# Kernel tuning notes

Measured on AMD Instinct MI355X. Metric: run time of the kernel, lower is better.

Reference implementation:

```python
import jax, jax.numpy as jnp
import numpy as np

N_NODES = 50000
N_EDGES = 800000
D = 256
VOCAB = 50000
N_ETYPES = 3
N_STEPS = 5
N_GRAPHS = 64


def setup_inputs() -> dict:
    key = jax.random.key(0)
    ks = jax.random.split(key, 16)
    s = 1.0 / np.sqrt(D)
    return {
        "x": jax.random.randint(ks[0], (N_NODES,), 0, VOCAB),
        "src": jax.random.randint(ks[1], (N_EDGES,), 0, N_NODES),
        "dst": jax.random.randint(ks[2], (N_EDGES,), 0, N_NODES),
        "etypes": jax.random.randint(ks[3], (N_EDGES,), 0, N_ETYPES),
        "seg_ids": jnp.sort(jax.random.randint(ks[4], (N_NODES,), 0, N_GRAPHS)),
        "num_graphs": N_GRAPHS,
        "emb": jax.random.normal(ks[5], (VOCAB, D), jnp.float32),
        "W_msg": jax.random.normal(ks[6], (N_ETYPES, D, D), jnp.float32) * s,
        "b_msg": jax.random.normal(ks[7], (N_ETYPES, D), jnp.float32) * s,
        "w_ih": jax.random.normal(ks[8], (3 * D, D), jnp.float32) * s,
        "w_hh": jax.random.normal(ks[9], (3 * D, D), jnp.float32) * s,
        "b_ih": jax.random.normal(ks[10], (3 * D,), jnp.float32) * s,
        "b_hh": jax.random.normal(ks[11], (3 * D,), jnp.float32) * s,
        "gate_w": jax.random.normal(ks[12], (D, 1), jnp.float32) * s,
        "gate_b": jax.random.normal(ks[13], (1,), jnp.float32) * s,
    }


def _gru_cell(a, h, w_ih, w_hh, b_ih, b_hh):
    # a, h: [N, D]; gates: [N, 3D]
    gi = a @ w_ih.T + b_ih
    gh = h @ w_hh.T + b_hh
    i_r, i_z, i_n = jnp.split(gi, 3, axis=-1)
    h_r, h_z, h_n = jnp.split(gh, 3, axis=-1)
    r = jax.nn.sigmoid(i_r + h_r)
    z = jax.nn.sigmoid(i_z + h_z)
    n = jnp.tanh(i_n + r * h_n)
    return (1.0 - z) * n + z * h


def reference(x, src, dst, etypes, seg_ids, num_graphs, emb, W_msg, b_msg,
              w_ih, w_hh, b_ih, b_hh, gate_w, gate_b):
    # Embedding lookup (dropout is identity in eval mode)
    h = emb[x]  # [N, D]

    # GatedGraphConv: n_steps of per-etype linear message + scatter-add + GRU
    for _ in range(N_STEPS):
        # per-node transform under every etype's weight: [n_etypes, N, D]
        t = jnp.einsum("nd,edf->enf", h, W_msg)
        msg = t[etypes, src] + b_msg[etypes]        # [E, D]
        a = jax.ops.segment_sum(msg, dst, num_segments=N_NODES)  # [N, D]
        h = _gru_cell(a, h, w_ih, w_hh, b_ih, b_hh)

    # GlobalAttentionPooling: gate score + segment softmax + weighted sum
    gate = (h @ gate_w + gate_b)[:, 0]  # [N]
    gmax = jax.ops.segment_max(gate, seg_ids, num_segments=num_graphs)
    e = jnp.exp(gate - gmax[seg_ids])
    denom = jax.ops.segment_sum(e, seg_ids, num_segments=num_graphs)
    alpha = e / denom[seg_ids]  # [N]
    out = jax.ops.segment_sum(h * alpha[:, None], seg_ids, num_segments=num_graphs)
    return out  # [num_graphs, D]
```

## Files before the change

### kernel.cpp

```cpp
#include <hip/hip_runtime.h>
#include <hip/hip_bf16.h>
#include <stdint.h>

#define N_NODESC 50000
#define NPAD     50048
#define N_EDGESC 800000
#define DIM      256
#define DIM3     768
#define NSTEPS   5
#define NGRAPH   64

typedef __attribute__((ext_vector_type(4))) float  f32x4;
typedef __attribute__((ext_vector_type(8))) short  short8;
typedef __attribute__((ext_vector_type(4))) unsigned short u16x4;
typedef __attribute__((ext_vector_type(4))) _Float16 f16x4;

__device__ float          g_hf[(size_t)NPAD * DIM];
__device__ unsigned short g_hb[(size_t)NPAD * DIM];
__device__ unsigned short g_p [(size_t)NPAD * DIM3];
__device__ unsigned short g_a [(size_t)NPAD * DIM];
__device__ _Float16       g_gi[(size_t)NPAD * DIM3];
__device__ _Float16       g_gh[(size_t)NPAD * DIM3];
__device__ unsigned short g_Wc[DIM * DIM3];
__device__ unsigned short g_WI[DIM3 * DIM];
__device__ unsigned short g_WH[DIM3 * DIM];
__device__ int            g_cnt[NPAD * 4];
__device__ int            g_rowoff[N_NODESC + 1];
__device__ int            g_cur[N_NODESC];
__device__ unsigned       g_eidx[N_EDGESC];
__device__ int            g_bsum[256];
__device__ int            g_boff[256];
__device__ float          g_gate[N_NODESC];
__device__ int            g_soff[NGRAPH + 1];
__device__ float          g_gmax[NGRAPH];
__device__ float          g_gden[NGRAPH];

__device__ __forceinline__ float bf2f(unsigned short u) {
  unsigned x = ((unsigned)u) << 16;
  return __builtin_bit_cast(float, x);
}
__device__ __forceinline__ unsigned short f2bf(float f) {
  unsigned u = __builtin_bit_cast(unsigned, f);
  u += 0x7fffu + ((u >> 16) & 1u);
  return (unsigned short)(u >> 16);
}
__device__ __forceinline__ float sigm(float x) { return 1.0f / (1.0f + expf(-x)); }

__device__ __forceinline__ void async16(const void* g, void* l) {
  __builtin_amdgcn_global_load_lds(
      (const __attribute__((address_space(1))) unsigned int*)g,
      (__attribute__((address_space(3))) unsigned int*)l, 16, 0, 0);
}


__global__ void k_zero_cnt() {
  int i = blockIdx.x * 256 + threadIdx.x;
  g_cnt[i] = 0;
}

__global__ void k_prep_w(const float* __restrict__ Wmsg, const float* __restrict__ wih,
                         const float* __restrict__ whh) {
  int i = blockIdx.x * 256 + threadIdx.x;
  if (i < 196608) {
    int f = i / 768, j = i - f * 768;
    int e = j >> 8, d = j & 255;
    g_Wc[i] = f2bf(Wmsg[(e << 16) + (d << 8) + f]);
  } else if (i < 393216) {
    int t = i - 196608;
    g_WI[t] = f2bf(wih[t]);
  } else if (i < 589824) {
    int t = i - 393216;
    g_WH[t] = f2bf(whh[t]);
  }
}

__global__ void k_embed(const int* __restrict__ x, const float* __restrict__ emb) {
  int i = blockIdx.x * 256 + threadIdx.x;
  int n = i >> 6, t = i & 63;
  if (n >= N_NODESC) return;
  float4 v = *(const float4*)(emb + (size_t)x[n] * DIM + t * 4);
  *(float4*)(g_hf + (size_t)n * DIM + t * 4) = v;
  u16x4 b = {f2bf(v.x), f2bf(v.y), f2bf(v.z), f2bf(v.w)};
  *(u16x4*)(g_hb + (size_t)n * DIM + t * 4) = b;
}

__global__ void k_count(const int* __restrict__ dst, const int* __restrict__ et) {
  int e = blockIdx.x * 256 + threadIdx.x;
  if (e >= N_EDGESC) return;
  atomicAdd(&g_cnt[dst[e] * 4 + et[e]], 1);
}

__global__ void k_scan1() {
  __shared__ int lds[256];
  int n = blockIdx.x * 256 + threadIdx.x;
  int deg = (n < N_NODESC) ? (g_cnt[n * 4] + g_cnt[n * 4 + 1] + g_cnt[n * 4 + 2]) : 0;
  lds[threadIdx.x] = deg;
  __syncthreads();
  for (int o = 128; o > 0; o >>= 1) {
    if (threadIdx.x < o) lds[threadIdx.x] += lds[threadIdx.x + o];
    __syncthreads();
  }
  if (threadIdx.x == 0) g_bsum[blockIdx.x] = lds[0];
}

__global__ void k_scan2() {
  __shared__ int lds[256];
  int t = threadIdx.x;
  int v = (t < 196) ? g_bsum[t] : 0;
  lds[t] = v;
  __syncthreads();
  for (int o = 1; o < 256; o <<= 1) {
    int u = (t >= o) ? lds[t - o] : 0;
    __syncthreads();
    lds[t] += u;
    __syncthreads();
  }
  if (t < 196) g_boff[t] = lds[t] - v;
}

__global__ void k_scan3() {
  __shared__ int lds[256];
  int n = blockIdx.x * 256 + threadIdx.x;
  int t = threadIdx.x;
  int deg = (n < N_NODESC) ? (g_cnt[n * 4] + g_cnt[n * 4 + 1] + g_cnt[n * 4 + 2]) : 0;
  lds[t] = deg;
  __syncthreads();
  for (int o = 1; o < 256; o <<= 1) {
    int u = (t >= o) ? lds[t - o] : 0;
    __syncthreads();
    lds[t] += u;
    __syncthreads();
  }
  if (n < N_NODESC) {
    int off = g_boff[blockIdx.x] + lds[t] - deg;
    g_rowoff[n] = off;
    g_cur[n] = off;
  }
  if (n == N_NODESC - 1) g_rowoff[N_NODESC] = g_boff[blockIdx.x] + lds[t];
}

__global__ void k_fill(const int* __restrict__ src, const int* __restrict__ dst,
                       const int* __restrict__ et) {
  int e = blockIdx.x * 256 + threadIdx.x;
  if (e >= N_EDGESC) return;
  int p = atomicAdd(&g_cur[dst[e]], 1);
  g_eidx[p] = (((unsigned)src[e]) << 2) | (unsigned)et[e];
}

__global__ void k_segoff(const int* __restrict__ seg) {
  int n = blockIdx.x * 256 + threadIdx.x;
  if (n >= N_NODESC) return;
  int g = seg[n];
  int gp = (n == 0) ? -1 : seg[n - 1];
  for (int t = gp + 1; t <= g; ++t) g_soff[t] = n;
  if (n == N_NODESC - 1)
    for (int t = g + 1; t <= NGRAPH; ++t) g_soff[t] = N_NODESC;
}


#define ACC_ET(hv, et)                                                        \
  {                                                                           \
    float x0 = bf2f(hv[0]), x1 = bf2f(hv[1]), x2 = bf2f(hv[2]), x3 = bf2f(hv[3]); \
    if (et == 0)      { a0[0] += x0; a0[1] += x1; a0[2] += x2; a0[3] += x3; } \
    else if (et == 1) { a1[0] += x0; a1[1] += x1; a1[2] += x2; a1[3] += x3; } \
    else              { a2[0] += x0; a2[1] += x1; a2[2] += x2; a2[3] += x3; } \
  }

__global__ __launch_bounds__(256) void k_agg() {
  int node = blockIdx.x * 4 + (threadIdx.x >> 6);
  int lane = threadIdx.x & 63;
  if (node >= N_NODESC) return;
  float a0[4] = {0.f, 0.f, 0.f, 0.f};
  float a1[4] = {0.f, 0.f, 0.f, 0.f};
  float a2[4] = {0.f, 0.f, 0.f, 0.f};
  int s = g_rowoff[node], e = g_rowoff[node + 1];
  int i = s;
  for (; i + 4 <= e; i += 4) {
    unsigned v0 = g_eidx[i], v1 = g_eidx[i + 1], v2 = g_eidx[i + 2], v3 = g_eidx[i + 3];
    u16x4 hv0 = *(const u16x4*)(g_hb + (size_t)(v0 >> 2) * DIM + lane * 4);
    u16x4 hv1 = *(const u16x4*)(g_hb + (size_t)(v1 >> 2) * DIM + lane * 4);
    u16x4 hv2 = *(const u16x4*)(g_hb + (size_t)(v2 >> 2) * DIM + lane * 4);
    u16x4 hv3 = *(const u16x4*)(g_hb + (size_t)(v3 >> 2) * DIM + lane * 4);
    int e0 = (int)(v0 & 3u), e1 = (int)(v1 & 3u), e2 = (int)(v2 & 3u), e3 = (int)(v3 & 3u);
    ACC_ET(hv0, e0);
    ACC_ET(hv1, e1);
    ACC_ET(hv2, e2);
    ACC_ET(hv3, e3);
  }
  for (; i < e; ++i) {
    unsigned v = g_eidx[i];
    u16x4 hv = *(const u16x4*)(g_hb + (size_t)(v >> 2) * DIM + lane * 4);
    int et = (int)(v & 3u);
    ACC_ET(hv, et);
  }
  size_t base = (size_t)node * DIM3 + lane * 4;
  u16x4 o0 = {f2bf(a0[0]), f2bf(a0[1]), f2bf(a0[2]), f2bf(a0[3])};
  u16x4 o1 = {f2bf(a1[0]), f2bf(a1[1]), f2bf(a1[2]), f2bf(a1[3])};
  u16x4 o2 = {f2bf(a2[0]), f2bf(a2[1]), f2bf(a2[2]), f2bf(a2[3])};
  *(u16x4*)(g_p + base)       = o0;
  *(u16x4*)(g_p + base + 256) = o1;
  *(u16x4*)(g_p + base + 512) = o2;
}

template <int MODE>
__global__ __launch_bounds__(256) void k_gemm(const float* __restrict__ bias,
                                              const float* __restrict__ bmsg) {
  constexpr int K  = (MODE == 0) ? DIM3 : DIM;
  constexpr int NC = (MODE == 0) ? DIM : DIM3;
  const unsigned short* __restrict__ A  = (MODE == 0) ? g_p  : (MODE == 1) ? g_a  : g_hb;
  const unsigned short* __restrict__ BT = (MODE == 0) ? g_Wc : (MODE == 1) ? g_WI : g_WH;

  __shared__ unsigned short lA[128 * 64];
  __shared__ unsigned short lB[128 * 64];
  const int tx = threadIdx.x;
  const int lane = tx & 63;
  const int wave = tx >> 6;
  const int wr = wave >> 1, wc = wave & 1;
  const int tileN = blockIdx.x * 128;
  const int tileM = blockIdx.y * 128;

  f32x4 acc[4][4];
#pragma unroll
  for (int m = 0; m < 4; ++m)
#pragma unroll
    for (int n = 0; n < 4; ++n) {
      acc[m][n][0] = 0.f; acc[m][n][1] = 0.f; acc[m][n][2] = 0.f; acc[m][n][3] = 0.f;
    }

  const int f  = lane & 15;
  const int q  = lane >> 4;
  const int xr = f & 7;

  int srow[4], scg[4];
#pragma unroll
  for (int i = 0; i < 4; ++i) {
    int byteo = i * 4096 + tx * 16;
    srow[i] = byteo >> 7;
    scg[i] = ((byteo >> 4) & 7) ^ (srow[i] & 7);
  }

  for (int k0 = 0; k0 < K; k0 += 64) {
#pragma unroll
    for (int i = 0; i < 4; ++i) {
      int byteo = i * 4096 + tx * 16;
      async16((const void*)(A + (size_t)(tileM + srow[i]) * K + k0 + scg[i] * 8),
              (void*)((char*)lA + byteo));
      async16((const void*)(BT + (size_t)(tileN + srow[i]) * K + k0 + scg[i] * 8),
              (void*)((char*)lB + byteo));
    }
    __syncthreads();
#pragma unroll
    for (int kk = 0; kk < 2; ++kk) {
      short8 af[4], bfr[4];
#pragma unroll
      for (int m = 0; m < 4; ++m)
        af[m] = *(const short8*)((const char*)lA +
                 (wr * 64 + m * 16 + f) * 128 + (((kk * 4 + q) ^ xr) * 16));
#pragma unroll
      for (int n = 0; n < 4; ++n)
        bfr[n] = *(const short8*)((const char*)lB +
                 (wc * 64 + n * 16 + f) * 128 + (((kk * 4 + q) ^ xr) * 16));
#pragma unroll
      for (int m = 0; m < 4; ++m)
#pragma unroll
        for (int n = 0; n < 4; ++n)
          acc[m][n] = __builtin_amdgcn_mfma_f32_16x16x32_bf16(af[m], bfr[n], acc[m][n], 0, 0, 0);
    }
    __syncthreads();
  }

#pragma unroll
  for (int m = 0; m < 4; ++m) {
    int row0 = tileM + wr * 64 + m * 16 + q * 4;
#pragma unroll
    for (int n = 0; n < 4; ++n) {
      int col = tileN + wc * 64 + n * 16 + f;
      f32x4 v = acc[m][n];
#pragma unroll
      for (int r = 0; r < 4; ++r) {
        int row = row0 + r;
        float val = v[r];
        if (MODE == 0) {
          const int* c = g_cnt + (size_t)row * 4;
          val += c[0] * bmsg[col] + c[1] * bmsg[256 + col] + c[2] * bmsg[512 + col];
          g_a[(size_t)row * NC + col] = f2bf(val);
        } else if (MODE == 1) {
          val += bias[col];
          g_gi[(size_t)row * NC + col] = (_Float16)val;
        } else {
          val += bias[col];
          g_gh[(size_t)row * NC + col] = (_Float16)val;
        }
      }
    }
  }
}

template <int LAST>
__global__ void k_gru(const float* __restrict__ gw, const float* __restrict__ gb) {
  int i = blockIdx.x * 256 + threadIdx.x;
  int n = i >> 6, t = (i & 63) * 4;
  if (n >= N_NODESC) return;
  size_t b3 = (size_t)n * DIM3 + t;
  size_t b1 = (size_t)n * DIM + t;
  f16x4 ir4 = *(const f16x4*)(g_gi + b3);
  f16x4 iz4 = *(const f16x4*)(g_gi + b3 + 256);
  f16x4 in4 = *(const f16x4*)(g_gi + b3 + 512);
  f16x4 hr4 = *(const f16x4*)(g_gh + b3);
  f16x4 hz4 = *(const f16x4*)(g_gh + b3 + 256);
  f16x4 hn4 = *(const f16x4*)(g_gh + b3 + 512);
  float4 h = *(const float4*)(g_hf + b1);
  float4 o;
#pragma unroll
  for (int j = 0; j < 4; ++j) {
    float r = sigm((float)ir4[j] + (float)hr4[j]);
    float z = sigm((float)iz4[j] + (float)hz4[j]);
    float nn = tanhf((float)in4[j] + r * (float)hn4[j]);
    float hj = (j == 0) ? h.x : (j == 1) ? h.y : (j == 2) ? h.z : h.w;
    float oj = (1.f - z) * nn + z * hj;
    if (j == 0) o.x = oj; else if (j == 1) o.y = oj; else if (j == 2) o.z = oj; else o.w = oj;
  }
  *(float4*)(g_hf + b1) = o;
  u16x4 ob = {f2bf(o.x), f2bf(o.y), f2bf(o.z), f2bf(o.w)};
  *(u16x4*)(g_hb + b1) = ob;
  if (LAST) {
    float4 w = *(const float4*)(gw + t);
    float p = o.x * w.x + o.y * w.y + o.z * w.z + o.w * w.w;
    for (int off = 32; off > 0; off >>= 1) p += __shfl_xor(p, off);
    if ((threadIdx.x & 63) == 0) g_gate[n] = p + gb[0];
  }
}


__global__ void k_segred() {
  int g = blockIdx.x, t = threadIdx.x;
  __shared__ float red[256];
  int s = g_soff[g], e = g_soff[g + 1];
  float m = -3.4e38f;
  for (int n = s + t; n < e; n += 256) m = fmaxf(m, g_gate[n]);
  red[t] = m;
  __syncthreads();
  for (int o = 128; o > 0; o >>= 1) {
    if (t < o) red[t] = fmaxf(red[t], red[t + o]);
    __syncthreads();
  }
  m = red[0];
  __syncthreads();
  float sm = 0.f;
  for (int n = s + t; n < e; n += 256) sm += expf(g_gate[n] - m);
  red[t] = sm;
  __syncthreads();
  for (int o = 128; o > 0; o >>= 1) {
    if (t < o) red[t] += red[t + o];
    __syncthreads();
  }
  if (t == 0) {
    g_gmax[g] = m;
    g_gden[g] = (e > s && red[0] != 0.f) ? red[0] : 1.f;
  }
}

__global__ void k_zero_out(float* __restrict__ out) {
  out[blockIdx.x * 256 + threadIdx.x] = 0.f;
}

__global__ __launch_bounds__(256) void k_poolacc(const int* __restrict__ seg,
                                                 float* __restrict__ out) {
  __shared__ int   segL[128];
  __shared__ float alphaL[128];
  int base = blockIdx.x * 128;
  int t = threadIdx.x;
  if (t < 128) {
    int n = base + t;
    if (n < N_NODESC) {
      int g = seg[n];
      segL[t] = g;
      alphaL[t] = expf(g_gate[n] - g_gmax[g]) / g_gden[g];
    } else {
      segL[t] = -1;
    }
  }
  __syncthreads();
  float acc = 0.f;
  int gcur = segL[0];
  for (int j = 0; j < 128; ++j) {
    int gs = segL[j];
    if (gs < 0) break;
    if (gs != gcur) {
      atomicAdd(out + (size_t)gcur * DIM + t, acc);
      acc = 0.f;
      gcur = gs;
    }
    acc += alphaL[j] * g_hf[(size_t)(base + j) * DIM + t];
  }
  if (gcur >= 0) atomicAdd(out + (size_t)gcur * DIM + t, acc);
}


extern "C" void kernel_launch(void* const* d_in, const int* in_sizes, int n_in,
                              void* d_out, int out_size, void* d_ws, size_t ws_size,
                              hipStream_t stream) {
  const int* x = (const int*)d_in[0];
  const int* src = (const int*)d_in[1];
  const int* dst = (const int*)d_in[2];
  const int* ety = (const int*)d_in[3];
  const int* seg = (const int*)d_in[4];
  const float* emb = (const float*)d_in[6];
  const float* Wmsg = (const float*)d_in[7];
  const float* bmsg = (const float*)d_in[8];
  const float* wih = (const float*)d_in[9];
  const float* whh = (const float*)d_in[10];
  const float* bih = (const float*)d_in[11];
  const float* bhh = (const float*)d_in[12];
  const float* gw = (const float*)d_in[13];
  const float* gb = (const float*)d_in[14];
  float* out = (float*)d_out;

  k_zero_cnt<<<NPAD * 4 / 256, 256, 0, stream>>>();
  k_prep_w<<<2304, 256, 0, stream>>>(Wmsg, wih, whh);
  k_embed<<<12500, 256, 0, stream>>>(x, emb);
  k_count<<<(N_EDGESC + 255) / 256, 256, 0, stream>>>(dst, ety);
  k_scan1<<<196, 256, 0, stream>>>();
  k_scan2<<<1, 256, 0, stream>>>();
  k_scan3<<<196, 256, 0, stream>>>();
  k_fill<<<(N_EDGESC + 255) / 256, 256, 0, stream>>>(src, dst, ety);
  k_segoff<<<196, 256, 0, stream>>>(seg);

  for (int s = 0; s < NSTEPS; ++s) {
    k_agg<<<12500, 256, 0, stream>>>();
    k_gemm<0><<<dim3(2, 391), 256, 0, stream>>>(nullptr, bmsg);
    k_gemm<1><<<dim3(6, 391), 256, 0, stream>>>(bih, nullptr);
    k_gemm<2><<<dim3(6, 391), 256, 0, stream>>>(bhh, nullptr);
    if (s < NSTEPS - 1)
      k_gru<0><<<12500, 256, 0, stream>>>(nullptr, nullptr);
    else
      k_gru<1><<<12500, 256, 0, stream>>>(gw, gb);
  }

  k_segred<<<NGRAPH, 256, 0, stream>>>();
  k_zero_out<<<NGRAPH, 256, 0, stream>>>(out);
  k_poolacc<<<391, 256, 0, stream>>>(seg, out);
}
```

Baseline: 1.576 ms.

## Double-buffer GEMM LDS tiles and merge independent message and hidden GEMMs

```diff
diff --git a/kernel.cpp b/kernel.cpp
--- a/kernel.cpp
+++ b/kernel.cpp
@@ -203,29 +203,21 @@
 }
 
 template <int MODE>
-__global__ __launch_bounds__(256) void k_gemm(const float* __restrict__ bias,
-                                              const float* __restrict__ bmsg) {
+__device__ __forceinline__ void gemm_body(unsigned short (*lA)[128 * 64],
+                                          unsigned short (*lB)[128 * 64],
+                                          const float* __restrict__ bias,
+                                          const float* __restrict__ bmsg,
+                                          int tileM, int tileN) {
   constexpr int K  = (MODE == 0) ? DIM3 : DIM;
   constexpr int NC = (MODE == 0) ? DIM : DIM3;
+  constexpr int NT = K / 64;
   const unsigned short* __restrict__ A  = (MODE == 0) ? g_p  : (MODE == 1) ? g_a  : g_hb;
   const unsigned short* __restrict__ BT = (MODE == 0) ? g_Wc : (MODE == 1) ? g_WI : g_WH;
 
-  __shared__ unsigned short lA[128 * 64];
-  __shared__ unsigned short lB[128 * 64];
   const int tx = threadIdx.x;
   const int lane = tx & 63;
   const int wave = tx >> 6;
   const int wr = wave >> 1, wc = wave & 1;
-  const int tileN = blockIdx.x * 128;
-  const int tileM = blockIdx.y * 128;
-
-  f32x4 acc[4][4];
-#pragma unroll
-  for (int m = 0; m < 4; ++m)
-#pragma unroll
-    for (int n = 0; n < 4; ++n) {
-      acc[m][n][0] = 0.f; acc[m][n][1] = 0.f; acc[m][n][2] = 0.f; acc[m][n][3] = 0.f;
-    }
 
   const int f  = lane & 15;
   const int q  = lane >> 4;
@@ -239,26 +231,41 @@
     scg[i] = ((byteo >> 4) & 7) ^ (srow[i] & 7);
   }
 
-  for (int k0 = 0; k0 < K; k0 += 64) {
+  auto STAGE = [&](int buf, int k0) {
 #pragma unroll
     for (int i = 0; i < 4; ++i) {
       int byteo = i * 4096 + tx * 16;
       async16((const void*)(A + (size_t)(tileM + srow[i]) * K + k0 + scg[i] * 8),
-              (void*)((char*)lA + byteo));
+              (void*)((char*)lA[buf] + byteo));
       async16((const void*)(BT + (size_t)(tileN + srow[i]) * K + k0 + scg[i] * 8),
-              (void*)((char*)lB + byteo));
-    }
-    __syncthreads();
+              (void*)((char*)lB[buf] + byteo));
+    }
+  };
+
+  f32x4 acc[4][4];
+#pragma unroll
+  for (int m = 0; m < 4; ++m)
+#pragma unroll
+    for (int n = 0; n < 4; ++n) {
+      acc[m][n][0] = 0.f; acc[m][n][1] = 0.f; acc[m][n][2] = 0.f; acc[m][n][3] = 0.f;
+    }
+
+  STAGE(0, 0);
+  __syncthreads();
+
+  int cur = 0;
+  for (int t = 0; t < NT; ++t) {
+    if (t + 1 < NT) STAGE(cur ^ 1, (t + 1) * 64);
 #pragma unroll
     for (int kk = 0; kk < 2; ++kk) {
       short8 af[4], bfr[4];
 #pragma unroll
       for (int m = 0; m < 4; ++m)
-        af[m] = *(const short8*)((const char*)lA +
+        af[m] = *(const short8*)((const char*)lA[cur] +
                  (wr * 64 + m * 16 + f) * 128 + (((kk * 4 + q) ^ xr) * 16));
 #pragma unroll
       for (int n = 0; n < 4; ++n)
-        bfr[n] = *(const short8*)((const char*)lB +
+        bfr[n] = *(const short8*)((const char*)lB[cur] +
                  (wc * 64 + n * 16 + f) * 128 + (((kk * 4 + q) ^ xr) * 16));
 #pragma unroll
       for (int m = 0; m < 4; ++m)
@@ -267,6 +274,7 @@
           acc[m][n] = __builtin_amdgcn_mfma_f32_16x16x32_bf16(af[m], bfr[n], acc[m][n], 0, 0, 0);
     }
     __syncthreads();
+    cur ^= 1;
   }
 
 #pragma unroll
@@ -294,6 +302,22 @@
       }
     }
   }
+}
+
+__global__ __launch_bounds__(256) void k_gemm02(const float* __restrict__ bmsg,
+                                                const float* __restrict__ bhh) {
+  __shared__ unsigned short lA[2][128 * 64];
+  __shared__ unsigned short lB[2][128 * 64];
+  if (blockIdx.x < 2)
+    gemm_body<0>(lA, lB, nullptr, bmsg, blockIdx.y * 128, blockIdx.x * 128);
+  else
+    gemm_body<2>(lA, lB, bhh, nullptr, blockIdx.y * 128, (blockIdx.x - 2) * 128);
+}
+
+__global__ __launch_bounds__(256) void k_gemm1(const float* __restrict__ bih) {
+  __shared__ unsigned short lA[2][128 * 64];
+  __shared__ unsigned short lB[2][128 * 64];
+  gemm_body<1>(lA, lB, bih, nullptr, blockIdx.y * 128, blockIdx.x * 128);
 }
 
 template <int LAST>
@@ -428,9 +452,8 @@
 
   for (int s = 0; s < NSTEPS; ++s) {
     k_agg<<<12500, 256, 0, stream>>>();
-    k_gemm<0><<<dim3(2, 391), 256, 0, stream>>>(nullptr, bmsg);
-    k_gemm<1><<<dim3(6, 391), 256, 0, stream>>>(bih, nullptr);
-    k_gemm<2><<<dim3(6, 391), 256, 0, stream>>>(bhh, nullptr);
+    k_gemm02<<<dim3(8, 391), 256, 0, stream>>>(bmsg, bhh);
+    k_gemm1<<<dim3(6, 391), 256, 0, stream>>>(bih);
     if (s < NSTEPS - 1)
       k_gru<0><<<12500, 256, 0, stream>>>(nullptr, nullptr);
     else
```

Result: slower. 1.938 ms (+23.0%).

## Co-schedule edge aggregation with hidden-state GEMM in one merged launch

Applied to the files above, without the earlier changes.

```diff
diff --git a/kernel.cpp b/kernel.cpp
--- a/kernel.cpp
+++ b/kernel.cpp
@@ -9,6 +9,9 @@
 #define DIM3     768
 #define NSTEPS   5
 #define NGRAPH   64
+
+#define AGG_BLOCKS  12500
+#define G2_BLOCKS   2346
 
 typedef __attribute__((ext_vector_type(4))) float  f32x4;
 typedef __attribute__((ext_vector_type(8))) short  short8;
@@ -166,8 +169,8 @@
     else              { a2[0] += x0; a2[1] += x1; a2[2] += x2; a2[3] += x3; } \
   }
 
-__global__ __launch_bounds__(256) void k_agg() {
-  int node = blockIdx.x * 4 + (threadIdx.x >> 6);
+__device__ __forceinline__ void agg_body(int nb) {
+  int node = nb * 4 + (threadIdx.x >> 6);
   int lane = threadIdx.x & 63;
   if (node >= N_NODESC) return;
   float a0[4] = {0.f, 0.f, 0.f, 0.f};
@@ -203,21 +206,19 @@
 }
 
 template <int MODE>
-__global__ __launch_bounds__(256) void k_gemm(const float* __restrict__ bias,
-                                              const float* __restrict__ bmsg) {
+__device__ __forceinline__ void gemm_body(unsigned short* lA, unsigned short* lB,
+                                          const float* __restrict__ bias,
+                                          const float* __restrict__ bmsg,
+                                          int tileM, int tileN) {
   constexpr int K  = (MODE == 0) ? DIM3 : DIM;
   constexpr int NC = (MODE == 0) ? DIM : DIM3;
   const unsigned short* __restrict__ A  = (MODE == 0) ? g_p  : (MODE == 1) ? g_a  : g_hb;
   const unsigned short* __restrict__ BT = (MODE == 0) ? g_Wc : (MODE == 1) ? g_WI : g_WH;
 
-  __shared__ unsigned short lA[128 * 64];
-  __shared__ unsigned short lB[128 * 64];
   const int tx = threadIdx.x;
   const int lane = tx & 63;
   const int wave = tx >> 6;
   const int wr = wave >> 1, wc = wave & 1;
-  const int tileN = blockIdx.x * 128;
-  const int tileM = blockIdx.y * 128;
 
   f32x4 acc[4][4];
 #pragma unroll
@@ -294,6 +295,32 @@
       }
     }
   }
+}
+
+__global__ __launch_bounds__(256) void k_agg_g2(const float* __restrict__ bhh) {
+  __shared__ unsigned short lA[128 * 64];
+  __shared__ unsigned short lB[128 * 64];
+  int g = blockIdx.x / 19, r = blockIdx.x % 19;
+  if (r < 16) {
+    int ab = g * 16 + r;
+    if (ab < AGG_BLOCKS) agg_body(ab);
+  } else {
+    int gb = g * 3 + (r - 16);
+    if (gb < G2_BLOCKS)
+      gemm_body<2>(lA, lB, bhh, nullptr, (gb / 6) * 128, (gb % 6) * 128);
+  }
+}
+
+__global__ __launch_bounds__(256) void k_gemm0(const float* __restrict__ bmsg) {
+  __shared__ unsigned short lA[128 * 64];
+  __shared__ unsigned short lB[128 * 64];
+  gemm_body<0>(lA, lB, nullptr, bmsg, blockIdx.y * 128, blockIdx.x * 128);
+}
+
+__global__ __launch_bounds__(256) void k_gemm1(const float* __restrict__ bih) {
+  __shared__ unsigned short lA[128 * 64];
+  __shared__ unsigned short lB[128 * 64];
+  gemm_body<1>(lA, lB, bih, nullptr, blockIdx.y * 128, blockIdx.x * 128);
 }
 
 template <int LAST>
@@ -426,11 +453,11 @@
   k_fill<<<(N_EDGESC + 255) / 256, 256, 0, stream>>>(src, dst, ety);
   k_segoff<<<196, 256, 0, stream>>>(seg);
 
+  const int MERGED = 782 * 19;
   for (int s = 0; s < NSTEPS; ++s) {
-    k_agg<<<12500, 256, 0, stream>>>();
-    k_gemm<0><<<dim3(2, 391), 256, 0, stream>>>(nullptr, bmsg);
-    k_gemm<1><<<dim3(6, 391), 256, 0, stream>>>(bih, nullptr);
-    k_gemm<2><<<dim3(6, 391), 256, 0, stream>>>(bhh, nullptr);
+    k_agg_g2<<<MERGED, 256, 0, stream>>>(bhh);
+    k_gemm0<<<dim3(2, 391), 256, 0, stream>>>(bmsg);
+    k_gemm1<<<dim3(6, 391), 256, 0, stream>>>(bih);
     if (s < NSTEPS - 1)
       k_gru<0><<<12500, 256, 0, stream>>>(nullptr, nullptr);
     else
```

Result: slower. 1.650 ms (+4.7%).

## Restructure GEMMs: full-width N tiles, merged gi/gh launch, weights read from global

Applied to the files above, without the earlier changes.

```diff
diff --git a/kernel.cpp b/kernel.cpp
--- a/kernel.cpp
+++ b/kernel.cpp
@@ -202,34 +202,22 @@
   *(u16x4*)(g_p + base + 512) = o2;
 }
 
-template <int MODE>
-__global__ __launch_bounds__(256) void k_gemm(const float* __restrict__ bias,
-                                              const float* __restrict__ bmsg) {
-  constexpr int K  = (MODE == 0) ? DIM3 : DIM;
-  constexpr int NC = (MODE == 0) ? DIM : DIM3;
-  const unsigned short* __restrict__ A  = (MODE == 0) ? g_p  : (MODE == 1) ? g_a  : g_hb;
-  const unsigned short* __restrict__ BT = (MODE == 0) ? g_Wc : (MODE == 1) ? g_WI : g_WH;
-
+__global__ __launch_bounds__(256) void k_gemm0(const float* __restrict__ bmsg) {
   __shared__ unsigned short lA[128 * 64];
-  __shared__ unsigned short lB[128 * 64];
   const int tx = threadIdx.x;
   const int lane = tx & 63;
   const int wave = tx >> 6;
   const int wr = wave >> 1, wc = wave & 1;
-  const int tileN = blockIdx.x * 128;
-  const int tileM = blockIdx.y * 128;
-
-  f32x4 acc[4][4];
+  const int tileM = blockIdx.x * 128;
+  const int f = lane & 15, q = lane >> 4, xr = f & 7;
+
+  f32x4 acc[4][8];
 #pragma unroll
   for (int m = 0; m < 4; ++m)
 #pragma unroll
-    for (int n = 0; n < 4; ++n) {
+    for (int n = 0; n < 8; ++n) {
       acc[m][n][0] = 0.f; acc[m][n][1] = 0.f; acc[m][n][2] = 0.f; acc[m][n][3] = 0.f;
     }
-
-  const int f  = lane & 15;
-  const int q  = lane >> 4;
-  const int xr = f & 7;
 
   int srow[4], scg[4];
 #pragma unroll
@@ -239,58 +227,117 @@
     scg[i] = ((byteo >> 4) & 7) ^ (srow[i] & 7);
   }
 
-  for (int k0 = 0; k0 < K; k0 += 64) {
+  for (int k0 = 0; k0 < DIM3; k0 += 64) {
 #pragma unroll
     for (int i = 0; i < 4; ++i) {
       int byteo = i * 4096 + tx * 16;
-      async16((const void*)(A + (size_t)(tileM + srow[i]) * K + k0 + scg[i] * 8),
+      async16((const void*)(g_p + (size_t)(tileM + srow[i]) * DIM3 + k0 + scg[i] * 8),
               (void*)((char*)lA + byteo));
-      async16((const void*)(BT + (size_t)(tileN + srow[i]) * K + k0 + scg[i] * 8),
-              (void*)((char*)lB + byteo));
     }
     __syncthreads();
 #pragma unroll
     for (int kk = 0; kk < 2; ++kk) {
-      short8 af[4], bfr[4];
+      short8 af[4], bfr[8];
 #pragma unroll
       for (int m = 0; m < 4; ++m)
         af[m] = *(const short8*)((const char*)lA +
                  (wr * 64 + m * 16 + f) * 128 + (((kk * 4 + q) ^ xr) * 16));
 #pragma unroll
-      for (int n = 0; n < 4; ++n)
-        bfr[n] = *(const short8*)((const char*)lB +
-                 (wc * 64 + n * 16 + f) * 128 + (((kk * 4 + q) ^ xr) * 16));
+      for (int n = 0; n < 8; ++n) {
+        int col = wc * 128 + n * 16 + f;
+        bfr[n] = *(const short8*)(g_Wc + (size_t)col * DIM3 + k0 + kk * 32 + q * 8);
+      }
+#pragma unroll
+      for (int m = 0; m < 4; ++m)
+#pragma unroll
+        for (int n = 0; n < 8; ++n)
+          acc[m][n] = __builtin_amdgcn_mfma_f32_16x16x32_bf16(af[m], bfr[n], acc[m][n], 0, 0, 0);
+    }
+    __syncthreads();
+  }
+
+#pragma unroll
+  for (int m = 0; m < 4; ++m) {
+    int row0 = tileM + wr * 64 + m * 16 + q * 4;
+#pragma unroll
+    for (int r = 0; r < 4; ++r) {
+      int row = row0 + r;
+      const int* c = g_cnt + (size_t)row * 4;
+      float c0 = (float)c[0], c1 = (float)c[1], c2 = (float)c[2];
+#pragma unroll
+      for (int n = 0; n < 8; ++n) {
+        int col = wc * 128 + n * 16 + f;
+        float val = acc[m][n][r] + c0 * bmsg[col] + c1 * bmsg[256 + col] + c2 * bmsg[512 + col];
+        g_a[(size_t)row * DIM + col] = f2bf(val);
+      }
+    }
+  }
+}
+
+__global__ __launch_bounds__(256) void k_gemm12(const float* __restrict__ bih,
+                                                const float* __restrict__ bhh) {
+  __shared__ unsigned short lA[128 * 256];
+  const int b = blockIdx.x;
+  const bool m1 = b < 391;
+  const int tileM = (m1 ? b : b - 391) * 128;
+  const unsigned short* __restrict__ A  = m1 ? g_a  : g_hb;
+  const unsigned short* __restrict__ BT = m1 ? g_WI : g_WH;
+  const float* __restrict__ bias = m1 ? bih : bhh;
+  _Float16* __restrict__ outp = m1 ? g_gi : g_gh;
+
+  const int tx = threadIdx.x;
+  const int lane = tx & 63;
+  const int wave = tx >> 6;
+  const int wr = wave >> 1, wc = wave & 1;
+  const int f = lane & 15, q = lane >> 4, xr = f & 7;
+
+#pragma unroll
+  for (int i = 0; i < 16; ++i) {
+    int byteo = i * 4096 + tx * 16;
+    int row = byteo >> 9;
+    int s = (byteo >> 4) & 31;
+    int cg = s ^ (row & 7);
+    async16((const void*)(A + (size_t)(tileM + row) * DIM + cg * 8),
+            (void*)((char*)lA + byteo));
+  }
+  __syncthreads();
+
+  for (int nt = 0; nt < 6; ++nt) {
+    f32x4 acc[4][4];
+#pragma unroll
+    for (int m = 0; m < 4; ++m)
+#pragma unroll
+      for (int n = 0; n < 4; ++n) {
+        acc[m][n][0] = 0.f; acc[m][n][1] = 0.f; acc[m][n][2] = 0.f; acc[m][n][3] = 0.f;
+      }
+#pragma unroll
+    for (int kk = 0; kk < 8; ++kk) {
+      short8 af[4], bfr[4];
+#pragma unroll
+      for (int m = 0; m < 4; ++m)
+        af[m] = *(const short8*)((const char*)lA +
+                 (wr * 64 + m * 16 + f) * 512 + (((kk * 4 + q) ^ xr) * 16));
+#pragma unroll
+      for (int n = 0; n < 4; ++n) {
+        int col = nt * 128 + wc * 64 + n * 16 + f;
+        bfr[n] = *(const short8*)(BT + (size_t)col * DIM + kk * 32 + q * 8);
+      }
 #pragma unroll
       for (int m = 0; m < 4; ++m)
 #pragma unroll
         for (int n = 0; n < 4; ++n)
           acc[m][n] = __builtin_amdgcn_mfma_f32_16x16x32_bf16(af[m], bfr[n], acc[m][n], 0, 0, 0);
     }
-    __syncthreads();
-  }
-
-#pragma unroll
-  for (int m = 0; m < 4; ++m) {
-    int row0 = tileM + wr * 64 + m * 16 + q * 4;
-#pragma unroll
-    for (int n = 0; n < 4; ++n) {
-      int col = tileN + wc * 64 + n * 16 + f;
-      f32x4 v = acc[m][n];
-#pragma unroll
-      for (int r = 0; r < 4; ++r) {
-        int row = row0 + r;
-        float val = v[r];
-        if (MODE == 0) {
-          const int* c = g_cnt + (size_t)row * 4;
-          val += c[0] * bmsg[col] + c[1] * bmsg[256 + col] + c[2] * bmsg[512 + col];
-          g_a[(size_t)row * NC + col] = f2bf(val);
-        } else if (MODE == 1) {
-          val += bias[col];
-          g_gi[(size_t)row * NC + col] = (_Float16)val;
-        } else {
-          val += bias[col];
-          g_gh[(size_t)row * NC + col] = (_Float16)val;
-        }
+#pragma unroll
+    for (int m = 0; m < 4; ++m) {
+      int row0 = tileM + wr * 64 + m * 16 + q * 4;
+#pragma unroll
+      for (int n = 0; n < 4; ++n) {
+        int col = nt * 128 + wc * 64 + n * 16 + f;
+        float bs = bias[col];
+#pragma unroll
+        for (int r = 0; r < 4; ++r)
+          outp[(size_t)(row0 + r) * DIM3 + col] = (_Float16)(acc[m][n][r] + bs);
       }
     }
   }
@@ -428,9 +475,8 @@
 
   for (int s = 0; s < NSTEPS; ++s) {
     k_agg<<<12500, 256, 0, stream>>>();
-    k_gemm<0><<<dim3(2, 391), 256, 0, stream>>>(nullptr, bmsg);
-    k_gemm<1><<<dim3(6, 391), 256, 0, stream>>>(bih, nullptr);
-    k_gemm<2><<<dim3(6, 391), 256, 0, stream>>>(bhh, nullptr);
+    k_gemm0<<<391, 256, 0, stream>>>(bmsg);
+    k_gemm12<<<782, 256, 0, stream>>>(bih, bhh);
     if (s < NSTEPS - 1)
       k_gru<0><<<12500, 256, 0, stream>>>(nullptr, nullptr);
     else
```

Result: slower. 1.875 ms (+19.0%).
